# Kernel optimization log

Hardware: AMD Instinct MI355X
Metric: run time of the kernel (lower is better)

Reference implementation:

```python
import jax, jax.numpy as jnp
import numpy as np

EPS = 1e-12  # matches torch F.normalize eps


def _l2_normalize(x):
    n = jnp.linalg.norm(x, axis=-1, keepdims=True)
    return x / jnp.maximum(n, EPS)


def setup_inputs() -> dict:
    key = jax.random.key(0)
    k1, k2, k3 = jax.random.split(key, 3)
    N, E, D = 100000, 1200000, 64
    feat = jax.random.normal(k1, (N, D), dtype=jnp.float32)
    beta = jnp.ones((1,), dtype=jnp.float32)
    src = jax.random.randint(k2, (E,), 0, N, dtype=jnp.int32)
    dst = jax.random.randint(k3, (E,), 0, N, dtype=jnp.int32)
    return {"feat": feat, "beta": beta, "src": src, "dst": dst}


def reference(feat, beta, src, dst):
    N = feat.shape[0]
    # cosine similarity on each edge (AGNN att_type)
    nh = _l2_normalize(feat)                                  # [N, D]
    e = beta[0] * jnp.sum(nh[src] * nh[dst], axis=-1)         # [E]
    # edge softmax over incoming edges of each destination node
    emax = jax.ops.segment_max(e, dst, num_segments=N)        # [N]
    emax = jnp.where(jnp.isfinite(emax), emax, 0.0)           # isolated nodes
    p = jnp.exp(e - emax[dst])                                # [E]
    psum = jax.ops.segment_sum(p, dst, num_segments=N)        # [N]
    p = p / jnp.maximum(psum[dst], EPS)                       # [E]
    # weighted scatter-sum aggregation: h_i' = sum_j p_ij * h_j
    msg = feat[src] * p[:, None]                              # [E, D]
    out = jax.ops.segment_sum(msg, dst, num_segments=N)       # [N, D]
    return out
```

## Files before the change

kernel.cpp:

```cpp
#include <hip/hip_runtime.h>
#include <hip/hip_fp16.h>

#define D 64
#define EPS 1e-12f
#define NPB 512
#define NPB_SHIFT 9
#define NB 256
#define CAP 8192
#define CAP_SHIFT 13
#define EPB 4096
#define SRC_BITS 17
#define CSRT 512

typedef _Float16 hv2 __attribute__((ext_vector_type(2)));

__device__ inline unsigned bc_u(__half2 h) { return __builtin_bit_cast(unsigned, h); }
__device__ inline __half2  bc_h(unsigned u) { return __builtin_bit_cast(__half2, u); }

__device__ inline float fdot2f(unsigned a, unsigned b, float c) {
#if defined(__has_builtin) && __has_builtin(__builtin_amdgcn_fdot2)
    return __builtin_amdgcn_fdot2(__builtin_bit_cast(hv2, a),
                                  __builtin_bit_cast(hv2, b), c, false);
#else
    __half2 ah = bc_h(a), bh = bc_h(b);
    return c + __low2float(ah) * __low2float(bh)
             + __high2float(ah) * __high2float(bh);
#endif
}

__global__ __launch_bounds__(1024) void scatter_nh_kernel(
        const int* __restrict__ src,
        const int* __restrict__ dst,
        const float4* __restrict__ feat4,
        int* __restrict__ bincursor,
        unsigned* __restrict__ pairs,
        float* __restrict__ norms,
        uint2* __restrict__ nh2,
        int N, int E, int nchunks) {
    __shared__ unsigned buf[EPB];
    __shared__ int hist[NB], offs[NB], cursor[NB], gbase[NB];
    __shared__ unsigned char binof[EPB];

    int tid = threadIdx.x;

    if ((int)blockIdx.x >= nchunks) {
        int gid = (blockIdx.x - nchunks) * 1024 + tid;
        if (gid >= N * 16) return;
        int row = gid >> 4, lg = gid & 15;
        float4 v = feat4[gid];
        float ss = v.x * v.x + v.y * v.y + v.z * v.z + v.w * v.w;
        #pragma unroll
        for (int off = 1; off < 16; off <<= 1) ss += __shfl_xor(ss, off, 64);
        float nrm = fmaxf(sqrtf(ss), EPS);
        float inv = 1.0f / nrm;
        if (lg == 0) norms[row] = nrm;
        uint2 p;
        p.x = bc_u(__floats2half2_rn(v.x * inv, v.y * inv));
        p.y = bc_u(__floats2half2_rn(v.z * inv, v.w * inv));
        nh2[gid] = p;
        return;
    }

    int base = blockIdx.x * EPB;
    int cnt  = min(EPB, E - base);
    int cnt4 = cnt >> 2;
    int tail = cnt & 3;

    if (tid < NB) hist[tid] = 0;
    __syncthreads();

    int4 dd4 = {0, 0, 0, 0};
    bool have = tid < cnt4;
    if (have) {
        dd4 = ((const int4*)(dst + base))[tid];
        atomicAdd(&hist[dd4.x >> NPB_SHIFT], 1);
        atomicAdd(&hist[dd4.y >> NPB_SHIFT], 1);
        atomicAdd(&hist[dd4.z >> NPB_SHIFT], 1);
        atomicAdd(&hist[dd4.w >> NPB_SHIFT], 1);
    }
    int dtail = 0;
    if (tid < tail) {
        dtail = dst[base + cnt4 * 4 + tid];
        atomicAdd(&hist[dtail >> NPB_SHIFT], 1);
    }
    __syncthreads();
    if (tid < 64) {
        int i0 = tid << 2;
        int h0 = hist[i0], h1 = hist[i0 + 1], h2 = hist[i0 + 2], h3 = hist[i0 + 3];
        int s = h0 + h1 + h2 + h3;
        int run = s;
        #pragma unroll
        for (int off = 1; off < 64; off <<= 1) {
            int nbr = __shfl_up(run, off, 64);
            if (tid >= off) run += nbr;
        }
        int acc = run - s;
        int hh[4] = {h0, h1, h2, h3};
        #pragma unroll
        for (int k = 0; k < 4; k++) {
            offs[i0 + k] = acc;
            cursor[i0 + k] = acc;
            if (hh[k] > 0)
                gbase[i0 + k] = ((i0 + k) << CAP_SHIFT)
                              + atomicAdd(&bincursor[i0 + k], hh[k]);
            acc += hh[k];
        }
    }
    __syncthreads();
    auto place = [&](int dd, int s) {
        int bb = dd >> NPB_SHIFT;
        int l = atomicAdd(&cursor[bb], 1);
        buf[l]   = ((unsigned)(dd & (NPB - 1)) << SRC_BITS) | (unsigned)s;
        binof[l] = (unsigned char)bb;
    };
    if (have) {
        int4 ss4 = ((const int4*)(src + base))[tid];
        place(dd4.x, ss4.x); place(dd4.y, ss4.y);
        place(dd4.z, ss4.z); place(dd4.w, ss4.w);
    }
    if (tid < tail) place(dtail, src[base + cnt4 * 4 + tid]);
    __syncthreads();
    for (int i = tid; i < cnt; i += 1024) {
        int b = binof[i];
        pairs[gbase[b] + (i - offs[b])] = buf[i];
    }
}

__global__ __launch_bounds__(CSRT) void csr_kernel(
        const unsigned* __restrict__ pairs,
        const int* __restrict__ bincursor,
        int* __restrict__ rowbeg,
        int* __restrict__ rowend,
        int* __restrict__ esrc,
        int N) {
    __shared__ unsigned buf[CAP];
    __shared__ int hist[NPB], cursor[NPB];

    int tid   = threadIdx.x;
    int b     = blockIdx.x;
    int base  = b << CAP_SHIFT;
    int cnt   = bincursor[b];
    int node0 = b << NPB_SHIFT;

    hist[tid] = 0;
    __syncthreads();
    int cnt4 = cnt >> 2;
    for (int i4 = tid; i4 < cnt4; i4 += CSRT) {
        uint4 p = ((const uint4*)(pairs + base))[i4];
        *(uint4*)&buf[i4 * 4] = p;
        atomicAdd(&hist[p.x >> SRC_BITS], 1);
        atomicAdd(&hist[p.y >> SRC_BITS], 1);
        atomicAdd(&hist[p.z >> SRC_BITS], 1);
        atomicAdd(&hist[p.w >> SRC_BITS], 1);
    }
    for (int i = cnt4 * 4 + tid; i < cnt; i += CSRT) {
        unsigned p = pairs[base + i];
        buf[i] = p;
        atomicAdd(&hist[p >> SRC_BITS], 1);
    }
    __syncthreads();
    if (tid < 64) {
        int i0 = tid << 3;
        int h[8], s = 0;
        #pragma unroll
        for (int k = 0; k < 8; k++) { h[k] = hist[i0 + k]; s += h[k]; }
        int run = s;
        #pragma unroll
        for (int off = 1; off < 64; off <<= 1) {
            int nbr = __shfl_up(run, off, 64);
            if (tid >= off) run += nbr;
        }
        int acc = run - s;
        #pragma unroll
        for (int k = 0; k < 8; k++) {
            cursor[i0 + k] = acc;
            int node = node0 + i0 + k;
            if (node < N) {
                rowbeg[node] = base + acc;
                rowend[node] = base + acc + h[k];
            }
            acc += h[k];
        }
    }
    __syncthreads();
    for (int i = tid; i < cnt; i += CSRT) {
        unsigned p = buf[i];
        int pos = atomicAdd(&cursor[p >> SRC_BITS], 1);
        esrc[base + pos] = (int)(p & ((1u << SRC_BITS) - 1));
    }
}

__global__ __launch_bounds__(256) void gather_kernel(const uint4* __restrict__ nh4,
                                                     const float* __restrict__ norms,
                                                     const float* __restrict__ beta_p,
                                                     const int* __restrict__ rowbeg,
                                                     const int* __restrict__ rowend,
                                                     const int* __restrict__ esrc,
                                                     float4* __restrict__ out4, int N) {
    int t    = blockIdx.x * 256 + threadIdx.x;
    int lane = threadIdx.x & 63;
    int g    = lane >> 3;
    int lg   = lane & 7;
    int d    = (t >> 6) * 8 + g;
    if (d >= N) return;

    int j   = rowbeg[d];
    int end = rowend[d];
    float beta = beta_p[0];

    uint4 fdp = nh4[(size_t)d * 8 + lg];

    __half2 acc0 = __float2half2_rn(0.f), acc1 = acc0, acc2 = acc0, acc3 = acc0;
    float ps = 0.f;

    for (; j < end; j += 4) {
        bool v1 = (j + 1 < end), v2 = (j + 2 < end), v3 = (j + 3 < end);
        int s0 = esrc[j];
        int s1 = v1 ? esrc[j + 1] : s0;
        int s2 = v2 ? esrc[j + 2] : s0;
        int s3 = v3 ? esrc[j + 3] : s0;
        uint4 p0 = nh4[(size_t)s0 * 8 + lg];
        uint4 p1 = nh4[(size_t)s1 * 8 + lg];
        uint4 p2 = nh4[(size_t)s2 * 8 + lg];
        uint4 p3 = nh4[(size_t)s3 * 8 + lg];
        float n0 = norms[s0], n1 = norms[s1], n2 = norms[s2], n3 = norms[s3];
        float d0 = fdot2f(p0.x, fdp.x, 0.f), d1 = fdot2f(p1.x, fdp.x, 0.f);
        float d2 = fdot2f(p2.x, fdp.x, 0.f), d3 = fdot2f(p3.x, fdp.x, 0.f);
        d0 = fdot2f(p0.y, fdp.y, d0); d1 = fdot2f(p1.y, fdp.y, d1);
        d2 = fdot2f(p2.y, fdp.y, d2); d3 = fdot2f(p3.y, fdp.y, d3);
        d0 = fdot2f(p0.z, fdp.z, d0); d1 = fdot2f(p1.z, fdp.z, d1);
        d2 = fdot2f(p2.z, fdp.z, d2); d3 = fdot2f(p3.z, fdp.z, d3);
        d0 = fdot2f(p0.w, fdp.w, d0); d1 = fdot2f(p1.w, fdp.w, d1);
        d2 = fdot2f(p2.w, fdp.w, d2); d3 = fdot2f(p3.w, fdp.w, d3);
        #pragma unroll
        for (int off = 1; off < 8; off <<= 1) {
            d0 += __shfl_xor(d0, off, 64);
            d1 += __shfl_xor(d1, off, 64);
            d2 += __shfl_xor(d2, off, 64);
            d3 += __shfl_xor(d3, off, 64);
        }
        float w0 = __expf(beta * d0);
        float w1 = v1 ? __expf(beta * d1) : 0.f;
        float w2 = v2 ? __expf(beta * d2) : 0.f;
        float w3 = v3 ? __expf(beta * d3) : 0.f;
        __half2 q0 = __float2half2_rn(w0 * n0);
        __half2 q1 = __float2half2_rn(w1 * n1);
        __half2 q2 = __float2half2_rn(w2 * n2);
        __half2 q3 = __float2half2_rn(w3 * n3);
        acc0 = __hfma2(q0, bc_h(p0.x), acc0); acc0 = __hfma2(q1, bc_h(p1.x), acc0);
        acc0 = __hfma2(q2, bc_h(p2.x), acc0); acc0 = __hfma2(q3, bc_h(p3.x), acc0);
        acc1 = __hfma2(q0, bc_h(p0.y), acc1); acc1 = __hfma2(q1, bc_h(p1.y), acc1);
        acc1 = __hfma2(q2, bc_h(p2.y), acc1); acc1 = __hfma2(q3, bc_h(p3.y), acc1);
        acc2 = __hfma2(q0, bc_h(p0.z), acc2); acc2 = __hfma2(q1, bc_h(p1.z), acc2);
        acc2 = __hfma2(q2, bc_h(p2.z), acc2); acc2 = __hfma2(q3, bc_h(p3.z), acc2);
        acc3 = __hfma2(q0, bc_h(p0.w), acc3); acc3 = __hfma2(q1, bc_h(p1.w), acc3);
        acc3 = __hfma2(q2, bc_h(p2.w), acc3); acc3 = __hfma2(q3, bc_h(p3.w), acc3);
        ps += w0 + w1 + w2 + w3;
    }

    float r = 1.0f / fmaxf(ps, EPS);
    float4 o0 = {__low2float(acc0) * r, __high2float(acc0) * r,
                 __low2float(acc1) * r, __high2float(acc1) * r};
    float4 o1 = {__low2float(acc2) * r, __high2float(acc2) * r,
                 __low2float(acc3) * r, __high2float(acc3) * r};
    out4[(size_t)d * 16 + lg * 2]     = o0;
    out4[(size_t)d * 16 + lg * 2 + 1] = o1;
}

extern "C" void kernel_launch(void* const* d_in, const int* in_sizes, int n_in,
                              void* d_out, int out_size, void* d_ws, size_t ws_size,
                              hipStream_t stream) {
    const float* feat = (const float*)d_in[0];
    const float* beta = (const float*)d_in[1];
    const int*   src  = (const int*)d_in[2];
    const int*   dst  = (const int*)d_in[3];

    int N = in_sizes[0] / D;
    int E = in_sizes[2];
    int nbins   = (N + NPB - 1) / NPB;
    int nchunks = (E + EPB - 1) / EPB;

    unsigned* pairs     = (unsigned*)d_ws;
    int*      esrc      = (int*)(pairs + (size_t)nbins * CAP);
    unsigned* nhraw     = (unsigned*)(esrc + (size_t)nbins * CAP);
    float*    norms     = (float*)(nhraw + (size_t)N * 32);
    int*      bincursor = (int*)(norms + N);
    int*      rowbeg    = bincursor + NB;
    int*      rowend    = rowbeg + N;

    (void)hipMemsetAsync(bincursor, 0, NB * sizeof(int), stream);

    int BI = (N * 16 + 1023) / 1024;
    scatter_nh_kernel<<<nchunks + BI, 1024, 0, stream>>>(
        src, dst, (const float4*)feat, bincursor, pairs, norms,
        (uint2*)nhraw, N, E, nchunks);
    csr_kernel<<<nbins, CSRT, 0, stream>>>(
        pairs, bincursor, rowbeg, rowend, esrc, N);
    gather_kernel<<<(N + 31) / 32, 256, 0, stream>>>(
        (const uint4*)nhraw, norms, beta, rowbeg, rowend, esrc,
        (float4*)d_out, N);
}
```

Before: 148.7 us.

## Split feature normalization across scatter and CSR kernels to fill idle CUs

Moves most of the per-node L2-normalize/fp16 packing blocks from the scatter kernel into the CSR kernel, launching them as extra blocks beyond the bin blocks. The scatter kernel keeps only enough normalize blocks to roughly fill two waves of the GPU. The CSR kernel is widened to 1024 threads. The aim is to overlap bandwidth-bound normalization with the underfilled CSR phase, at the cost of larger per-block footprint and possible contention with CSR's atomics.

```diff
diff --git a/kernel.cpp b/kernel.cpp
--- a/kernel.cpp
+++ b/kernel.cpp
@@ -10,7 +10,6 @@
 #define CAP_SHIFT 13
 #define EPB 4096
 #define SRC_BITS 17
-#define CSRT 512
 
 typedef _Float16 hv2 __attribute__((ext_vector_type(2)));
 
@@ -26,6 +25,24 @@
     return c + __low2float(ah) * __low2float(bh)
              + __high2float(ah) * __high2float(bh);
 #endif
+}
+
+__device__ inline void nh_body(const float4* __restrict__ feat4,
+                               float* __restrict__ norms,
+                               uint2* __restrict__ nh2, int gid, int N) {
+    if (gid >= N * 16) return;
+    int row = gid >> 4, lg = gid & 15;
+    float4 v = feat4[gid];
+    float ss = v.x * v.x + v.y * v.y + v.z * v.z + v.w * v.w;
+    #pragma unroll
+    for (int off = 1; off < 16; off <<= 1) ss += __shfl_xor(ss, off, 64);
+    float nrm = fmaxf(sqrtf(ss), EPS);
+    float inv = 1.0f / nrm;
+    if (lg == 0) norms[row] = nrm;
+    uint2 p;
+    p.x = bc_u(__floats2half2_rn(v.x * inv, v.y * inv));
+    p.y = bc_u(__floats2half2_rn(v.z * inv, v.w * inv));
+    nh2[gid] = p;
 }
 
 __global__ __launch_bounds__(1024) void scatter_nh_kernel(
@@ -44,20 +61,7 @@
     int tid = threadIdx.x;
 
     if ((int)blockIdx.x >= nchunks) {
-        int gid = (blockIdx.x - nchunks) * 1024 + tid;
-        if (gid >= N * 16) return;
-        int row = gid >> 4, lg = gid & 15;
-        float4 v = feat4[gid];
-        float ss = v.x * v.x + v.y * v.y + v.z * v.z + v.w * v.w;
-        #pragma unroll
-        for (int off = 1; off < 16; off <<= 1) ss += __shfl_xor(ss, off, 64);
-        float nrm = fmaxf(sqrtf(ss), EPS);
-        float inv = 1.0f / nrm;
-        if (lg == 0) norms[row] = nrm;
-        uint2 p;
-        p.x = bc_u(__floats2half2_rn(v.x * inv, v.y * inv));
-        p.y = bc_u(__floats2half2_rn(v.z * inv, v.w * inv));
-        nh2[gid] = p;
+        nh_body(feat4, norms, nh2, (blockIdx.x - nchunks) * 1024 + tid, N);
         return;
     }
 
@@ -126,26 +130,36 @@
     }
 }
 
-__global__ __launch_bounds__(CSRT) void csr_kernel(
+__global__ __launch_bounds__(1024) void csr_nh_kernel(
         const unsigned* __restrict__ pairs,
         const int* __restrict__ bincursor,
         int* __restrict__ rowbeg,
         int* __restrict__ rowend,
         int* __restrict__ esrc,
-        int N) {
+        const float4* __restrict__ feat4,
+        float* __restrict__ norms,
+        uint2* __restrict__ nh2,
+        int N, int nbins, int nh1) {
     __shared__ unsigned buf[CAP];
     __shared__ int hist[NPB], cursor[NPB];
 
-    int tid   = threadIdx.x;
+    int tid = threadIdx.x;
+
+    if ((int)blockIdx.x >= nbins) {
+        nh_body(feat4, norms, nh2,
+                (nh1 + (int)blockIdx.x - nbins) * 1024 + tid, N);
+        return;
+    }
+
     int b     = blockIdx.x;
     int base  = b << CAP_SHIFT;
     int cnt   = bincursor[b];
     int node0 = b << NPB_SHIFT;
 
-    hist[tid] = 0;
+    if (tid < NPB) hist[tid] = 0;
     __syncthreads();
     int cnt4 = cnt >> 2;
-    for (int i4 = tid; i4 < cnt4; i4 += CSRT) {
+    for (int i4 = tid; i4 < cnt4; i4 += 1024) {
         uint4 p = ((const uint4*)(pairs + base))[i4];
         *(uint4*)&buf[i4 * 4] = p;
         atomicAdd(&hist[p.x >> SRC_BITS], 1);
@@ -153,7 +167,7 @@
         atomicAdd(&hist[p.z >> SRC_BITS], 1);
         atomicAdd(&hist[p.w >> SRC_BITS], 1);
     }
-    for (int i = cnt4 * 4 + tid; i < cnt; i += CSRT) {
+    for (int i = cnt4 * 4 + tid; i < cnt; i += 1024) {
         unsigned p = pairs[base + i];
         buf[i] = p;
         atomicAdd(&hist[p >> SRC_BITS], 1);
@@ -183,7 +197,7 @@
         }
     }
     __syncthreads();
-    for (int i = tid; i < cnt; i += CSRT) {
+    for (int i = tid; i < cnt; i += 1024) {
         unsigned p = buf[i];
         int pos = atomicAdd(&cursor[p >> SRC_BITS], 1);
         esrc[base + pos] = (int)(p & ((1u << SRC_BITS) - 1));
@@ -290,12 +304,18 @@
 
     (void)hipMemsetAsync(bincursor, 0, NB * sizeof(int), stream);
 
-    int BI = (N * 16 + 1023) / 1024;
-    scatter_nh_kernel<<<nchunks + BI, 1024, 0, stream>>>(
+    int BI  = (N * 16 + 1023) / 1024;
+    int nh1 = 2 * 256 - nchunks;
+    if (nh1 < 0) nh1 = 0;
+    if (nh1 > BI) nh1 = BI;
+    int nh2 = BI - nh1;
+
+    scatter_nh_kernel<<<nchunks + nh1, 1024, 0, stream>>>(
         src, dst, (const float4*)feat, bincursor, pairs, norms,
         (uint2*)nhraw, N, E, nchunks);
-    csr_kernel<<<nbins, CSRT, 0, stream>>>(
-        pairs, bincursor, rowbeg, rowend, esrc, N);
+    csr_nh_kernel<<<nbins + nh2, 1024, 0, stream>>>(
+        pairs, bincursor, rowbeg, rowend, esrc,
+        (const float4*)feat, norms, (uint2*)nhraw, N, nbins, nh1);
     gather_kernel<<<(N + 31) / 32, 256, 0, stream>>>(
         (const uint4*)nhraw, norms, beta, rowbeg, rowend, esrc,
         (float4*)d_out, N);
```

Result: no change. 146.3 us (-1.6%).
